# Optimization experiments

Hardware: AMD Instinct MI355X
Metric: run time of the kernel (lower is better)

Reference implementation:

```python
import jax, jax.numpy as jnp
import numpy as np

B, S, H, NH = 4, 2048, 2048, 16
HD = H // NH  # 128
CAUSAL = True


def setup_inputs() -> dict:
    key = jax.random.key(0)
    ks = jax.random.split(key, 5)
    mk = lambda k: jax.random.normal(k, (H, H), dtype=jnp.float32) * 0.02
    return {
        "x": jax.random.normal(ks[0], (B, S, H), dtype=jnp.float32),
        "w_q": mk(ks[1]),
        "w_k": mk(ks[2]),
        "w_v": mk(ks[3]),
        "w_o": mk(ks[4]),
    }


def reference(x, w_q, w_k, w_v, w_o):
    b, s, _ = x.shape
    # QKV projections (x @ W.T), split into heads: [b, nh, s, hd]
    q = (x @ w_q.T).reshape(b, s, NH, HD).transpose(0, 2, 1, 3)
    k = (x @ w_k.T).reshape(b, s, NH, HD).transpose(0, 2, 1, 3)
    v = (x @ w_v.T).reshape(b, s, NH, HD).transpose(0, 2, 1, 3)
    scale = 1.0 / jnp.sqrt(jnp.asarray(HD, dtype=x.dtype))
    score = jnp.einsum('bhqd,bhkd->bhqk', q, k) * scale  # [b, nh, s, s]
    if CAUSAL:
        mask = jnp.triu(jnp.ones((s, s), dtype=bool), k=1)
        score = jnp.where(mask, -jnp.inf, score)
    attn = jax.nn.softmax(score, axis=-1)
    o = jnp.einsum('bhqk,bhkd->bhqd', attn, v)  # [b, nh, s, hd]
    o = o.transpose(0, 2, 1, 3).reshape(b, s, H)
    return o @ w_o.T
```

## Files before the change

kernel.cpp:

```cpp
#include <hip/hip_runtime.h>

#define S_LEN 2048
#define HSZ   2048
#define M_TOK 8192

typedef float f32x4 __attribute__((ext_vector_type(4)));
typedef __bf16 bf16x8 __attribute__((ext_vector_type(8)));
typedef __bf16 bf16x4 __attribute__((ext_vector_type(4)));

typedef __attribute__((address_space(3))) __bf16 lds_bf16_t;
typedef __attribute__((address_space(1))) const __bf16 glb_bf16_t;

__device__ __forceinline__ void async16(__bf16* ldst, const __bf16* gsrc) {
    __builtin_amdgcn_global_load_lds((glb_bf16_t*)gsrc, (lds_bf16_t*)ldst, 16, 0, 0);
}

#define MFMA16(a, b, c) __builtin_amdgcn_mfma_f32_16x16x32_bf16((a), (b), (c), 0, 0, 0)

__global__ void cast_f32_bf16(const float* __restrict__ s, __bf16* __restrict__ d, int n4) {
    int idx = blockIdx.x * blockDim.x + threadIdx.x;
    int stride = gridDim.x * blockDim.x;
    for (int i = idx; i < n4; i += stride) {
        float4 v = ((const float4*)s)[i];
        bf16x4 o = { (__bf16)v.x, (__bf16)v.y, (__bf16)v.z, (__bf16)v.w };
        ((bf16x4*)d)[i] = o;
    }
}

__global__ void cast_weights(const float* __restrict__ wq, const float* __restrict__ wk,
                             const float* __restrict__ wv, const float* __restrict__ wo,
                             __bf16* __restrict__ wqkvb, __bf16* __restrict__ wob,
                             int n4seg) {
    int idx = blockIdx.x * blockDim.x + threadIdx.x;
    int stride = gridDim.x * blockDim.x;
    int total = 4 * n4seg;
    for (int i = idx; i < total; i += stride) {
        int seg = i / n4seg;
        int off = i - seg * n4seg;
        const float* s = (seg == 0) ? wq : (seg == 1) ? wk : (seg == 2) ? wv : wo;
        __bf16* d = (seg < 3) ? (wqkvb + (size_t)seg * n4seg * 4) : wob;
        float4 v = ((const float4*)s)[off];
        bf16x4 o = { (__bf16)v.x, (__bf16)v.y, (__bf16)v.z, (__bf16)v.w };
        ((bf16x4*)d)[off] = o;
    }
}

template <typename CT>
__global__ __launch_bounds__(256) void gemm_bt(const __bf16* __restrict__ A,
                                               const __bf16* __restrict__ B,
                                               CT* __restrict__ C,
                                               int M, int N, int K) {
    __shared__ __bf16 As[2 * 128 * 32];
    __shared__ __bf16 Bs[2 * 128 * 32];

    const int tid  = threadIdx.x;
    const int w    = tid >> 6;
    const int lane = tid & 63;
    const int quad = lane >> 4;
    const int l15  = lane & 15;

    const int m0 = blockIdx.y * 128;
    const int n0 = blockIdx.x * 128;
    const int wr = (w & 1) * 64;
    const int wc = (w >> 1) * 64;

    f32x4 acc[4][4] = {};

    for (int k0 = 0; k0 < K; k0 += 64) {
        __syncthreads();
        #pragma unroll
        for (int i = 0; i < 4; ++i) {
            int e  = (w * 4 + i) * 512 + lane * 8;
            int kc = e >> 12, r = (e >> 5) & 127, c = e & 31;
            async16(&As[e], &A[(size_t)(m0 + r) * K + k0 + kc * 32 + c]);
            async16(&Bs[e], &B[(size_t)(n0 + r) * K + k0 + kc * 32 + c]);
        }
        __syncthreads();

        #pragma unroll
        for (int ks = 0; ks < 2; ++ks) {
            bf16x8 af[4], bfr[4];
            #pragma unroll
            for (int mi = 0; mi < 4; ++mi)
                af[mi] = *(const bf16x8*)&As[ks * 4096 + (wr + mi * 16 + l15) * 32 + quad * 8];
            #pragma unroll
            for (int ni = 0; ni < 4; ++ni)
                bfr[ni] = *(const bf16x8*)&Bs[ks * 4096 + (wc + ni * 16 + l15) * 32 + quad * 8];
            #pragma unroll
            for (int mi = 0; mi < 4; ++mi)
                #pragma unroll
                for (int ni = 0; ni < 4; ++ni)
                    acc[mi][ni] = MFMA16(af[mi], bfr[ni], acc[mi][ni]);
        }
    }

    #pragma unroll
    for (int mi = 0; mi < 4; ++mi)
        #pragma unroll
        for (int ni = 0; ni < 4; ++ni)
            #pragma unroll
            for (int i = 0; i < 4; ++i) {
                int r = m0 + wr + mi * 16 + quad * 4 + i;
                int c = n0 + wc + ni * 16 + l15;
                C[(size_t)r * N + c] = (CT)acc[mi][ni][i];
            }
}

__global__ __launch_bounds__(256) void gemm_qkv(const __bf16* __restrict__ A,
                                                const __bf16* __restrict__ B,
                                                __bf16* __restrict__ Qo,
                                                __bf16* __restrict__ Ko,
                                                __bf16* __restrict__ VT,
                                                int M, int N, int K) {
    __shared__ __bf16 As[2 * 128 * 32];
    __shared__ __bf16 Bs[2 * 128 * 32];

    const int tid  = threadIdx.x;
    const int w    = tid >> 6;
    const int lane = tid & 63;
    const int quad = lane >> 4;
    const int l15  = lane & 15;

    const int m0 = blockIdx.y * 128;
    const int n0 = blockIdx.x * 128;
    const int wr = (w & 1) * 64;
    const int wc = (w >> 1) * 64;

    f32x4 acc[4][4] = {};

    for (int k0 = 0; k0 < K; k0 += 64) {
        __syncthreads();
        #pragma unroll
        for (int i = 0; i < 4; ++i) {
            int e  = (w * 4 + i) * 512 + lane * 8;
            int kc = e >> 12, r = (e >> 5) & 127, c = e & 31;
            async16(&As[e], &A[(size_t)(m0 + r) * K + k0 + kc * 32 + c]);
            async16(&Bs[e], &B[(size_t)(n0 + r) * K + k0 + kc * 32 + c]);
        }
        __syncthreads();

        #pragma unroll
        for (int ks = 0; ks < 2; ++ks) {
            bf16x8 af[4], bfr[4];
            #pragma unroll
            for (int mi = 0; mi < 4; ++mi)
                af[mi] = *(const bf16x8*)&As[ks * 4096 + (wr + mi * 16 + l15) * 32 + quad * 8];
            #pragma unroll
            for (int ni = 0; ni < 4; ++ni)
                bfr[ni] = *(const bf16x8*)&Bs[ks * 4096 + (wc + ni * 16 + l15) * 32 + quad * 8];
            #pragma unroll
            for (int mi = 0; mi < 4; ++mi)
                #pragma unroll
                for (int ni = 0; ni < 4; ++ni)
                    acc[mi][ni] = MFMA16(af[mi], bfr[ni], acc[mi][ni]);
        }
    }

    const int seg = n0 >> 11;
    const int nn  = n0 & 2047;

    if (seg < 2) {
        __bf16* Cv = seg ? Ko : Qo;
        #pragma unroll
        for (int mi = 0; mi < 4; ++mi)
            #pragma unroll
            for (int ni = 0; ni < 4; ++ni)
                #pragma unroll
                for (int i = 0; i < 4; ++i) {
                    int r = m0 + wr + mi * 16 + quad * 4 + i;
                    int c = nn + wc + ni * 16 + l15;
                    Cv[(size_t)r * HSZ + c] = (__bf16)acc[mi][ni][i];
                }
    } else {
        #pragma unroll
        for (int mi = 0; mi < 4; ++mi)
            #pragma unroll
            for (int ni = 0; ni < 4; ++ni) {
                int r0 = m0 + wr + mi * 16 + quad * 4;
                int c  = nn + wc + ni * 16 + l15;
                int bb = r0 >> 11;
                int s  = r0 & 2047;
                size_t base = ((size_t)(bb * 2048 + c) << 11) + s;
                bf16x4 v = { (__bf16)acc[mi][ni][0], (__bf16)acc[mi][ni][1],
                             (__bf16)acc[mi][ni][2], (__bf16)acc[mi][ni][3] };
                *(bf16x4*)&VT[base] = v;
            }
    }
}

__global__ __launch_bounds__(256, 2) void flash_fwd(const __bf16* __restrict__ Q,
                                                    const __bf16* __restrict__ K,
                                                    const __bf16* __restrict__ VT,
                                                    __bf16* __restrict__ O) {
    const int bx = blockIdx.x;
    const int qt = 15 - (bx >> 6);
    const int bh = bx & 63;
    const int q0 = qt * 128;

    const int tid  = threadIdx.x;
    const int w    = tid >> 6;
    const int lane = tid & 63;
    const int quad = lane >> 4;
    const int l15  = lane & 15;

    __shared__ __bf16 Ks[4 * 64 * 32];
    __shared__ __bf16 Vt[2 * 128 * 32];
    __shared__ __bf16 Ps[2 * 128 * 40];

    const int bq = bh >> 4, hh = bh & 15;
    const size_t base = ((size_t)bq * S_LEN) * HSZ + (size_t)hh * 128;
    const __bf16* Qg  = Q + base + (size_t)q0 * HSZ;
    const __bf16* VTg = VT + (size_t)bh * 128 * 2048;

    bf16x8 qf[2][4];
    #pragma unroll
    for (int mb = 0; mb < 2; ++mb)
        #pragma unroll
        for (int ks = 0; ks < 4; ++ks)
            qf[mb][ks] = *(const bf16x8*)&Qg[(size_t)(w * 32 + mb * 16 + l15) * HSZ + ks * 32 + quad * 8];

    f32x4 o_acc[2][8] = {};
    f32x4 psum[2] = {};

    const float scl = 0.08838834764831845f * 1.4426950408889634f;
    const float CC  = 8.0f * 1.4426950408889634f;
    bf16x8 ones;
    #pragma unroll
    for (int j = 0; j < 8; ++j) ones[j] = (__bf16)1.0f;

    const int n_kv = 2 * qt + 2;
    for (int kvt = 0; kvt < n_kv; ++kvt) {
        const int k0r = kvt * 64;
        __syncthreads();

        const __bf16* Kg = K + base + (size_t)k0r * HSZ;
        #pragma unroll
        for (int i = 0; i < 4; ++i) {
            int e  = (w * 4 + i) * 512 + lane * 8;
            int kc = e >> 11, r = (e >> 5) & 63, c = e & 31;
            async16(&Ks[e], &Kg[(size_t)r * HSZ + kc * 32 + c]);
        }
        #pragma unroll
        for (int i = 0; i < 4; ++i) {
            int e   = (w * 4 + i) * 512 + lane * 8;
            int kvc = e >> 12, dd = (e >> 5) & 127, c = e & 31;
            async16(&Vt[e], &VTg[(size_t)dd * 2048 + k0r + kvc * 32 + c]);
        }
        __syncthreads();

        f32x4 s_acc[2][4] = {};
        #pragma unroll
        for (int ks = 0; ks < 4; ++ks)
            #pragma unroll
            for (int nt = 0; nt < 4; ++nt) {
                bf16x8 bk = *(const bf16x8*)&Ks[ks * 2048 + (nt * 16 + l15) * 32 + quad * 8];
                s_acc[0][nt] = MFMA16(qf[0][ks], bk, s_acc[0][nt]);
                s_acc[1][nt] = MFMA16(qf[1][ks], bk, s_acc[1][nt]);
            }

        if (kvt >= 2 * qt) {
            #pragma unroll
            for (int mb = 0; mb < 2; ++mb) {
                int row = q0 + w * 32 + mb * 16 + quad * 4;
                #pragma unroll
                for (int nt = 0; nt < 4; ++nt) {
                    int col = k0r + nt * 16 + l15;
                    #pragma unroll
                    for (int i = 0; i < 4; ++i)
                        if (col > row + i) s_acc[mb][nt][i] = -1e30f;
                }
            }
        }

        #pragma unroll
        for (int mb = 0; mb < 2; ++mb)
            #pragma unroll
            for (int nt = 0; nt < 4; ++nt)
                #pragma unroll
                for (int i = 0; i < 4; ++i) {
                    float p = exp2f(s_acc[mb][nt][i] * scl - CC);
                    Ps[(nt >> 1) * 5120 + (w * 32 + mb * 16 + quad * 4 + i) * 40 + (nt & 1) * 16 + l15] = (__bf16)p;
                }

        #pragma unroll
        for (int ks2 = 0; ks2 < 2; ++ks2) {
            bf16x8 ap0 = *(const bf16x8*)&Ps[ks2 * 5120 + (w * 32 + l15) * 40 + quad * 8];
            bf16x8 ap1 = *(const bf16x8*)&Ps[ks2 * 5120 + (w * 32 + 16 + l15) * 40 + quad * 8];
            psum[0] = MFMA16(ap0, ones, psum[0]);
            psum[1] = MFMA16(ap1, ones, psum[1]);
            #pragma unroll
            for (int nt = 0; nt < 8; ++nt) {
                bf16x8 bv = *(const bf16x8*)&Vt[ks2 * 4096 + (nt * 16 + l15) * 32 + quad * 8];
                o_acc[0][nt] = MFMA16(ap0, bv, o_acc[0][nt]);
                o_acc[1][nt] = MFMA16(ap1, bv, o_acc[1][nt]);
            }
        }
    }

    __bf16* Og = O + base + (size_t)q0 * HSZ;
    #pragma unroll
    for (int mb = 0; mb < 2; ++mb)
        #pragma unroll
        for (int i = 0; i < 4; ++i) {
            float inv = 1.f / psum[mb][i];
            int r = w * 32 + mb * 16 + quad * 4 + i;
            #pragma unroll
            for (int nt = 0; nt < 8; ++nt)
                Og[(size_t)r * HSZ + nt * 16 + l15] = (__bf16)(o_acc[mb][nt][i] * inv);
        }
}

extern "C" void kernel_launch(void* const* d_in, const int* in_sizes, int n_in,
                              void* d_out, int out_size, void* d_ws, size_t ws_size,
                              hipStream_t stream) {
    const float* x  = (const float*)d_in[0];
    const float* wq = (const float*)d_in[1];
    const float* wk = (const float*)d_in[2];
    const float* wv = (const float*)d_in[3];
    const float* wo = (const float*)d_in[4];
    float* out = (float*)d_out;

    const size_t nX = (size_t)M_TOK * HSZ;
    const size_t nW = (size_t)HSZ * HSZ;

    char* ws = (char*)d_ws;
    __bf16* xb    = (__bf16*)ws;  ws += nX * 2;
    __bf16* wqkvb = (__bf16*)ws;  ws += 3 * nW * 2;
    __bf16* wob   = (__bf16*)ws;  ws += nW * 2;
    __bf16* Qb    = (__bf16*)ws;  ws += nX * 2;
    __bf16* Kb    = (__bf16*)ws;  ws += nX * 2;
    __bf16* VTb   = (__bf16*)ws;  ws += nX * 2;
    __bf16* Ob    = (__bf16*)ws;  ws += nX * 2;

    cast_f32_bf16<<<2048, 256, 0, stream>>>(x, xb, (int)(nX / 4));
    cast_weights<<<2048, 256, 0, stream>>>(wq, wk, wv, wo, wqkvb, wob, (int)(nW / 4));

    dim3 gq(3 * HSZ / 128, M_TOK / 128);
    gemm_qkv<<<gq, 256, 0, stream>>>(xb, wqkvb, Qb, Kb, VTb, M_TOK, 3 * HSZ, HSZ);

    flash_fwd<<<64 * (S_LEN / 128), 256, 0, stream>>>(Qb, Kb, VTb, Ob);

    dim3 gg(HSZ / 128, M_TOK / 128);
    gemm_bt<float><<<gg, 256, 0, stream>>>(Ob, wob, out, M_TOK, HSZ, HSZ);
}
```

Before: 564.4 us.

## Replace GEMMs with 256x256 double-buffered swizzled-LDS pipelined kernel

```diff
diff --git a/kernel.cpp b/kernel.cpp
--- a/kernel.cpp
+++ b/kernel.cpp
@@ -45,147 +45,171 @@
     }
 }
 
-template <typename CT>
-__global__ __launch_bounds__(256) void gemm_bt(const __bf16* __restrict__ A,
-                                               const __bf16* __restrict__ B,
-                                               CT* __restrict__ C,
-                                               int M, int N, int K) {
-    __shared__ __bf16 As[2 * 128 * 32];
-    __shared__ __bf16 Bs[2 * 128 * 32];
-
-    const int tid  = threadIdx.x;
-    const int w    = tid >> 6;
-    const int lane = tid & 63;
-    const int quad = lane >> 4;
-    const int l15  = lane & 15;
-
-    const int m0 = blockIdx.y * 128;
-    const int n0 = blockIdx.x * 128;
-    const int wr = (w & 1) * 64;
-    const int wc = (w >> 1) * 64;
-
-    f32x4 acc[4][4] = {};
-
-    for (int k0 = 0; k0 < K; k0 += 64) {
-        __syncthreads();
-        #pragma unroll
-        for (int i = 0; i < 4; ++i) {
-            int e  = (w * 4 + i) * 512 + lane * 8;
-            int kc = e >> 12, r = (e >> 5) & 127, c = e & 31;
-            async16(&As[e], &A[(size_t)(m0 + r) * K + k0 + kc * 32 + c]);
-            async16(&Bs[e], &B[(size_t)(n0 + r) * K + k0 + kc * 32 + c]);
-        }
-        __syncthreads();
-
-        #pragma unroll
-        for (int ks = 0; ks < 2; ++ks) {
-            bf16x8 af[4], bfr[4];
-            #pragma unroll
-            for (int mi = 0; mi < 4; ++mi)
-                af[mi] = *(const bf16x8*)&As[ks * 4096 + (wr + mi * 16 + l15) * 32 + quad * 8];
-            #pragma unroll
-            for (int ni = 0; ni < 4; ++ni)
-                bfr[ni] = *(const bf16x8*)&Bs[ks * 4096 + (wc + ni * 16 + l15) * 32 + quad * 8];
-            #pragma unroll
-            for (int mi = 0; mi < 4; ++mi)
-                #pragma unroll
-                for (int ni = 0; ni < 4; ++ni)
-                    acc[mi][ni] = MFMA16(af[mi], bfr[ni], acc[mi][ni]);
-        }
-    }
-
-    #pragma unroll
-    for (int mi = 0; mi < 4; ++mi)
-        #pragma unroll
-        for (int ni = 0; ni < 4; ++ni)
-            #pragma unroll
-            for (int i = 0; i < 4; ++i) {
-                int r = m0 + wr + mi * 16 + quad * 4 + i;
-                int c = n0 + wc + ni * 16 + l15;
-                C[(size_t)r * N + c] = (CT)acc[mi][ni][i];
-            }
-}
-
-__global__ __launch_bounds__(256) void gemm_qkv(const __bf16* __restrict__ A,
-                                                const __bf16* __restrict__ B,
-                                                __bf16* __restrict__ Qo,
-                                                __bf16* __restrict__ Ko,
-                                                __bf16* __restrict__ VT,
-                                                int M, int N, int K) {
-    __shared__ __bf16 As[2 * 128 * 32];
-    __shared__ __bf16 Bs[2 * 128 * 32];
-
-    const int tid  = threadIdx.x;
-    const int w    = tid >> 6;
-    const int lane = tid & 63;
-    const int quad = lane >> 4;
-    const int l15  = lane & 15;
-
-    const int m0 = blockIdx.y * 128;
-    const int n0 = blockIdx.x * 128;
-    const int wr = (w & 1) * 64;
-    const int wc = (w >> 1) * 64;
-
-    f32x4 acc[4][4] = {};
-
-    for (int k0 = 0; k0 < K; k0 += 64) {
-        __syncthreads();
-        #pragma unroll
-        for (int i = 0; i < 4; ++i) {
-            int e  = (w * 4 + i) * 512 + lane * 8;
-            int kc = e >> 12, r = (e >> 5) & 127, c = e & 31;
-            async16(&As[e], &A[(size_t)(m0 + r) * K + k0 + kc * 32 + c]);
-            async16(&Bs[e], &B[(size_t)(n0 + r) * K + k0 + kc * 32 + c]);
-        }
-        __syncthreads();
-
-        #pragma unroll
-        for (int ks = 0; ks < 2; ++ks) {
-            bf16x8 af[4], bfr[4];
-            #pragma unroll
-            for (int mi = 0; mi < 4; ++mi)
-                af[mi] = *(const bf16x8*)&As[ks * 4096 + (wr + mi * 16 + l15) * 32 + quad * 8];
-            #pragma unroll
-            for (int ni = 0; ni < 4; ++ni)
-                bfr[ni] = *(const bf16x8*)&Bs[ks * 4096 + (wc + ni * 16 + l15) * 32 + quad * 8];
-            #pragma unroll
-            for (int mi = 0; mi < 4; ++mi)
-                #pragma unroll
-                for (int ni = 0; ni < 4; ++ni)
-                    acc[mi][ni] = MFMA16(af[mi], bfr[ni], acc[mi][ni]);
-        }
-    }
+
+#define G_BAR() __builtin_amdgcn_s_barrier()
+#define LGKM0() do { asm volatile("s_waitcnt lgkmcnt(0)" ::: "memory"); \
+                     __builtin_amdgcn_sched_barrier(0); } while (0)
+#define VMC(n)  do { asm volatile("s_waitcnt vmcnt(" #n ")" ::: "memory"); \
+                     __builtin_amdgcn_sched_barrier(0); } while (0)
+
+#define STAGE_A(bsel, kofs, half) do { \
+    const __bf16* gp_ = A + (size_t)m0 * K + (kofs); \
+    __bf16* sp_ = sm + (bsel) * 32768; \
+    _Pragma("unroll") \
+    for (int i_ = 0; i_ < 2; ++i_) { \
+        int g_ = (w * 2 + i_) * 64 + lane; \
+        int ri_ = g_ >> 3, c16_ = g_ & 7; \
+        int row_ = (half) * 64 + (ri_ & 63) + (ri_ >> 6) * 128; \
+        async16(&sp_[row_ * 64 + c16_ * 8], \
+                &gp_[(size_t)row_ * K + ((c16_ ^ (row_ & 7)) * 8)]); \
+    } } while (0)
+
+#define STAGE_B(bsel, kofs, half) do { \
+    const __bf16* gp_ = Bm + (size_t)n0 * K + (kofs); \
+    __bf16* sp_ = sm + (bsel) * 32768 + 16384; \
+    _Pragma("unroll") \
+    for (int i_ = 0; i_ < 2; ++i_) { \
+        int g_ = (w * 2 + i_) * 64 + lane; \
+        int ri_ = g_ >> 3, c16_ = g_ & 7; \
+        int row_ = (half) * 32 + (ri_ & 31) + (ri_ >> 5) * 64; \
+        async16(&sp_[row_ * 64 + c16_ * 8], \
+                &gp_[(size_t)row_ * K + ((c16_ ^ (row_ & 7)) * 8)]); \
+    } } while (0)
+
+#define LOAD_A(bsel, qm) do { \
+    const __bf16* ap_ = sm + (bsel) * 32768; \
+    _Pragma("unroll") \
+    for (int mi_ = 0; mi_ < 4; ++mi_) { \
+        int R_ = wm * 128 + (qm) * 64 + mi_ * 16 + l15; \
+        int sw_ = (R_ & 7) << 3; \
+        af[mi_][0] = *(const bf16x8*)&ap_[R_ * 64 + ((quad * 8) ^ sw_)]; \
+        af[mi_][1] = *(const bf16x8*)&ap_[R_ * 64 + ((32 + quad * 8) ^ sw_)]; \
+    } } while (0)
+
+#define LOAD_B(bsel, qn, dst) do { \
+    const __bf16* bp_ = sm + (bsel) * 32768 + 16384; \
+    _Pragma("unroll") \
+    for (int ni_ = 0; ni_ < 2; ++ni_) { \
+        int R_ = wn * 64 + (qn) * 32 + ni_ * 16 + l15; \
+        int sw_ = (R_ & 7) << 3; \
+        dst[ni_][0] = *(const bf16x8*)&bp_[R_ * 64 + ((quad * 8) ^ sw_)]; \
+        dst[ni_][1] = *(const bf16x8*)&bp_[R_ * 64 + ((32 + quad * 8) ^ sw_)]; \
+    } } while (0)
+
+#define MFMA_Q(qm, qn, bsrc) do { \
+    __builtin_amdgcn_s_setprio(1); \
+    _Pragma("unroll") \
+    for (int mi_ = 0; mi_ < 4; ++mi_) \
+        _Pragma("unroll") \
+        for (int ni_ = 0; ni_ < 2; ++ni_) { \
+            acc[(qm) * 4 + mi_][(qn) * 2 + ni_] = \
+                MFMA16(af[mi_][0], bsrc[ni_][0], acc[(qm) * 4 + mi_][(qn) * 2 + ni_]); \
+            acc[(qm) * 4 + mi_][(qn) * 2 + ni_] = \
+                MFMA16(af[mi_][1], bsrc[ni_][1], acc[(qm) * 4 + mi_][(qn) * 2 + ni_]); \
+        } \
+    __builtin_amdgcn_s_setprio(0); \
+} while (0)
+
+#define GEMM256_MAIN() \
+    const int w = threadIdx.x >> 6, lane = threadIdx.x & 63; \
+    const int wm = w >> 2, wn = w & 3; \
+    const int quad = lane >> 4, l15 = lane & 15; \
+    const int m0 = blockIdx.y * 256, n0 = blockIdx.x * 256; \
+    f32x4 acc[8][4] = {}; \
+    bf16x8 af[4][2], b0f[2][2], b1f[2][2]; \
+    const int NT = K >> 6; \
+     \
+    STAGE_A(0, 0, 0); STAGE_B(0, 0, 1); STAGE_A(0, 0, 1); STAGE_B(0, 0, 0); \
+    STAGE_A(1, 64, 0); STAGE_B(1, 64, 1); \
+    VMC(4); \
+    G_BAR(); \
+    _Pragma("unroll 2") \
+    for (int kt = 0; kt < NT; ++kt) { \
+        const int buf = kt & 1, nbuf = buf ^ 1; \
+        const int k1 = (kt + 1) << 6, k2 = (kt + 2) << 6; \
+         \
+        LOAD_A(buf, 0); \
+        LOAD_B(buf, 0, b0f); \
+        if (kt + 1 < NT) STAGE_A(nbuf, k1, 1); \
+        G_BAR(); LGKM0(); \
+        MFMA_Q(0, 0, b0f); \
+        G_BAR(); \
+         \
+        LOAD_B(buf, 1, b1f); \
+        if (kt + 1 < NT) STAGE_B(nbuf, k1, 0); \
+        G_BAR(); LGKM0(); \
+        MFMA_Q(0, 1, b1f); \
+        G_BAR(); \
+         \
+        LOAD_A(buf, 1); \
+        if (kt + 2 < NT) STAGE_A(buf, k2, 0); \
+        G_BAR(); LGKM0(); \
+        MFMA_Q(1, 1, b1f); \
+        G_BAR(); \
+         \
+        if (kt + 2 < NT) STAGE_B(buf, k2, 1); \
+        G_BAR(); \
+        MFMA_Q(1, 0, b0f); \
+        if (kt + 2 < NT) { VMC(4); } else if (kt + 1 < NT) { VMC(0); } \
+        G_BAR(); \
+    }
+
+__global__ __launch_bounds__(512, 2) void gemm_qkv8(const __bf16* __restrict__ A,
+                                                    const __bf16* __restrict__ Bm,
+                                                    __bf16* __restrict__ Qo,
+                                                    __bf16* __restrict__ Ko,
+                                                    __bf16* __restrict__ VT,
+                                                    int K) {
+    __shared__ __bf16 sm[65536];
+    GEMM256_MAIN();
 
     const int seg = n0 >> 11;
-    const int nn  = n0 & 2047;
-
+    const int nn  = (n0 & 2047) + wn * 64;
     if (seg < 2) {
         __bf16* Cv = seg ? Ko : Qo;
         #pragma unroll
-        for (int mi = 0; mi < 4; ++mi)
+        for (int mi = 0; mi < 8; ++mi)
             #pragma unroll
             for (int ni = 0; ni < 4; ++ni)
                 #pragma unroll
                 for (int i = 0; i < 4; ++i) {
-                    int r = m0 + wr + mi * 16 + quad * 4 + i;
-                    int c = nn + wc + ni * 16 + l15;
+                    int r = m0 + wm * 128 + mi * 16 + quad * 4 + i;
+                    int c = nn + ni * 16 + l15;
                     Cv[(size_t)r * HSZ + c] = (__bf16)acc[mi][ni][i];
                 }
     } else {
         #pragma unroll
-        for (int mi = 0; mi < 4; ++mi)
+        for (int mi = 0; mi < 8; ++mi)
             #pragma unroll
             for (int ni = 0; ni < 4; ++ni) {
-                int r0 = m0 + wr + mi * 16 + quad * 4;
-                int c  = nn + wc + ni * 16 + l15;
-                int bb = r0 >> 11;
-                int s  = r0 & 2047;
+                int r0 = m0 + wm * 128 + mi * 16 + quad * 4;
+                int c  = nn + ni * 16 + l15;
+                int bb = r0 >> 11, s = r0 & 2047;
                 size_t base = ((size_t)(bb * 2048 + c) << 11) + s;
                 bf16x4 v = { (__bf16)acc[mi][ni][0], (__bf16)acc[mi][ni][1],
                              (__bf16)acc[mi][ni][2], (__bf16)acc[mi][ni][3] };
                 *(bf16x4*)&VT[base] = v;
             }
     }
+}
+
+__global__ __launch_bounds__(512, 2) void gemm_out(const __bf16* __restrict__ A,
+                                                   const __bf16* __restrict__ Bm,
+                                                   float* __restrict__ C,
+                                                   int K) {
+    __shared__ __bf16 sm[65536];
+    GEMM256_MAIN();
+
+    #pragma unroll
+    for (int mi = 0; mi < 8; ++mi)
+        #pragma unroll
+        for (int ni = 0; ni < 4; ++ni)
+            #pragma unroll
+            for (int i = 0; i < 4; ++i) {
+                int r = m0 + wm * 128 + mi * 16 + quad * 4 + i;
+                int c = n0 + wn * 64 + ni * 16 + l15;
+                C[(size_t)r * HSZ + c] = acc[mi][ni][i];
+            }
 }
 
 __global__ __launch_bounds__(256, 2) void flash_fwd(const __bf16* __restrict__ Q,
@@ -335,11 +359,11 @@
     cast_f32_bf16<<<2048, 256, 0, stream>>>(x, xb, (int)(nX / 4));
     cast_weights<<<2048, 256, 0, stream>>>(wq, wk, wv, wo, wqkvb, wob, (int)(nW / 4));
 
-    dim3 gq(3 * HSZ / 128, M_TOK / 128);
-    gemm_qkv<<<gq, 256, 0, stream>>>(xb, wqkvb, Qb, Kb, VTb, M_TOK, 3 * HSZ, HSZ);
+    dim3 gq(3 * HSZ / 256, M_TOK / 256);
+    gemm_qkv8<<<gq, 512, 0, stream>>>(xb, wqkvb, Qb, Kb, VTb, HSZ);
 
     flash_fwd<<<64 * (S_LEN / 128), 256, 0, stream>>>(Qb, Kb, VTb, Ob);
 
-    dim3 gg(HSZ / 128, M_TOK / 128);
-    gemm_bt<float><<<gg, 256, 0, stream>>>(Ob, wob, out, M_TOK, HSZ, HSZ);
-}
+    dim3 gg(HSZ / 256, M_TOK / 256);
+    gemm_out<<<gg, 512, 0, stream>>>(Ob, wob, out, HSZ);
+}
```

New measurement: 514.3 us. -8.9%, faster.
